# Kernel tuning notes

Hardware: AMD Instinct MI355X
Metric: run time of the kernel (lower is better)

## Reference

```python
import jax, jax.numpy as jnp
import numpy as np

B, N, M, D = 2, 256, 8, 256      # batch, seq, modalities, dmodel
H, DH = 8, 64                     # heads, dim_head (hardcoded defaults)
INNER = H * DH                    # 512
MULT = 4                          # FFN mult
SCALE = DH ** -0.5
EPS = 1e-5


def layer_norm(x, g, b):
    mu = jnp.mean(x, axis=-1, keepdims=True)
    var = jnp.mean((x - mu) ** 2, axis=-1, keepdims=True)
    return (x - mu) * jax.lax.rsqrt(var + EPS) * g + b


def setup_inputs() -> dict:
    key = jax.random.key(0)
    ks = jax.random.split(key, 8)
    s = 0.02
    return {
        "x": jax.random.normal(ks[0], (B, D, M, N), jnp.float32),
        "Wq": jax.random.normal(ks[1], (D, INNER), jnp.float32) * s,
        "Wkv": jax.random.normal(ks[2], (D, 2 * INNER), jnp.float32) * s,
        "Wout": jax.random.normal(ks[3], (INNER * M, D * M), jnp.float32) * s,
        "bout": jnp.zeros((D * M,), jnp.float32),
        "g1": jnp.ones((D,), jnp.float32),
        "beta1": jnp.zeros((D,), jnp.float32),
        "Wff1": jax.random.normal(ks[4], (D, 2 * D * MULT), jnp.float32) * s,
        "bff1": jnp.zeros((2 * D * MULT,), jnp.float32),
        "Wff2": jax.random.normal(ks[5], (D * MULT, D), jnp.float32) * s,
        "bff2": jnp.zeros((D,), jnp.float32),
        "g2": jnp.ones((D,), jnp.float32),
        "beta2": jnp.zeros((D,), jnp.float32),
    }


def reference(x, Wq, Wkv, Wout, bout, g1, beta1, Wff1, bff1, Wff2, bff2, g2, beta2):
    x_shape = x.shape
    xt = jnp.transpose(x, (0, 3, 2, 1))          # [B,N,M,D]
    # --- Channel_Seq_Big_Attention (self-attention, context = x) ---
    q = (xt @ Wq).reshape(B, N, M, H, DH)
    kv = xt @ Wkv
    k, v = jnp.split(kv, 2, axis=-1)
    k = k.reshape(B, N, M, H, DH)
    v = v.reshape(B, N, M, H, DH)
    # sim: [(b h), i, j, m, z] kept as [B,H,i,j,m,z]
    sim = jnp.einsum('bimhd,bjzhd->bhijmz', q, k) * SCALE
    attn = jax.nn.softmax(sim, axis=2)           # softmax over j (dim=-3 of bijmz)
    out = jnp.einsum('bhijmz,bjmhd->bizhd', attn, v)  # [B,N,M,H,DH]
    out = out.reshape(B, N, M * H * DH)          # 'b n (m h d)'
    o = (out @ Wout + bout).reshape(B, N, M, D)
    # --- residual + post-norm ---
    xt = layer_norm(xt + o, g1, beta1)
    # --- GEGLU FFN ---
    hg = xt @ Wff1 + bff1
    a, gate = jnp.split(hg, 2, axis=-1)
    ff = (a * jax.nn.gelu(gate, approximate=False)) @ Wff2 + bff2
    xt = layer_norm(xt + ff, g2, beta2)
    return xt.reshape(x_shape)                   # torch .view(x_shape)
```

## Files before the change

### kernel.cpp

```cpp
#include <hip/hip_runtime.h>
#include <math.h>

#define SCALE_ 0.125f
#define KS_ 0.1803368801111244f

typedef __attribute__((ext_vector_type(8))) short bf16x8;
typedef __attribute__((ext_vector_type(4))) short bf16x4;
typedef __attribute__((ext_vector_type(4))) float f32x4;

__device__ inline short f2bf(float f) {
  unsigned u = __builtin_bit_cast(unsigned, f);
  u += 0x7fff + ((u >> 16) & 1);
  return (short)(u >> 16);
}

__global__ __launch_bounds__(256) void k_transpose(const float* __restrict__ x, float* __restrict__ xt,
                                                   short* __restrict__ xtbf) {
  __shared__ float tile[32][33];
  int bm = blockIdx.z; int b = bm >> 3; int m = bm & 7;
  int d0 = blockIdx.x * 32, n0 = blockIdx.y * 32;
#pragma unroll
  for (int r = 0; r < 32; r += 8) {
    int d = d0 + threadIdx.y + r, n = n0 + threadIdx.x;
    tile[threadIdx.y + r][threadIdx.x] = x[((size_t)(b * 256 + d) * 8 + m) * 256 + n];
  }
  __syncthreads();
#pragma unroll
  for (int r = 0; r < 32; r += 8) {
    int n = n0 + threadIdx.y + r, d = d0 + threadIdx.x;
    float v = tile[threadIdx.x][threadIdx.y + r];
    size_t idx = ((size_t)(b * 256 + n) * 8 + m) * 256 + d;
    xt[idx] = v;
    xtbf[idx] = f2bf(v);
  }
}

__global__ __launch_bounds__(256) void k_wt(const float* __restrict__ W, short* __restrict__ WT, int K, int N) {
  __shared__ float tile[32][33];
  int n0 = blockIdx.x * 32, k0 = blockIdx.y * 32;
  int tx = threadIdx.x & 31, ty = threadIdx.x >> 5;
#pragma unroll
  for (int r = 0; r < 32; r += 8)
    tile[ty + r][tx] = W[(size_t)(k0 + ty + r) * N + n0 + tx];
  __syncthreads();
#pragma unroll
  for (int r = 0; r < 32; r += 8)
    WT[(size_t)(n0 + ty + r) * K + k0 + tx] = f2bf(tile[tx][ty + r]);
}

__global__ __launch_bounds__(256) void k_gemm_bf(const short* __restrict__ A, const short* __restrict__ Bt,
                                                 const float* __restrict__ bias, float* __restrict__ C,
                                                 int M, int N, int K, int Ks) {
  __shared__ short As[64 * 40];
  __shared__ short Bs[64 * 40];
  int t = threadIdx.x;
  int row0 = blockIdx.y * 64, col0 = blockIdx.x * 64;
  int kp = blockIdx.z;
  int kbeg = kp * Ks, kend = kbeg + Ks;
  int w = t >> 6, lane = t & 63, quad = lane >> 4, l16 = lane & 15;
  int wr = w >> 1, wc = w & 1;
  int lrow = t >> 2, lch = (t & 3) * 8;
  const short* Ap = A + (size_t)(row0 + lrow) * K + lch;
  const short* Bp = Bt + (size_t)(col0 + lrow) * K + lch;
  f32x4 acc[2][2] = {{{0,0,0,0},{0,0,0,0}},{{0,0,0,0},{0,0,0,0}}};
  bf16x8 av = *(const bf16x8*)(Ap + kbeg);
  bf16x8 bv = *(const bf16x8*)(Bp + kbeg);
  for (int k0 = kbeg; k0 < kend; k0 += 32) {
    *(bf16x8*)&As[lrow * 40 + lch] = av;
    *(bf16x8*)&Bs[lrow * 40 + lch] = bv;
    __syncthreads();
    if (k0 + 32 < kend) {
      av = *(const bf16x8*)(Ap + k0 + 32);
      bv = *(const bf16x8*)(Bp + k0 + 32);
    }
    bf16x8 af[2], bf[2];
#pragma unroll
    for (int rf = 0; rf < 2; rf++) af[rf] = *(const bf16x8*)&As[(wr * 32 + rf * 16 + l16) * 40 + quad * 8];
#pragma unroll
    for (int cf = 0; cf < 2; cf++) bf[cf] = *(const bf16x8*)&Bs[(wc * 32 + cf * 16 + l16) * 40 + quad * 8];
#pragma unroll
    for (int rf = 0; rf < 2; rf++)
#pragma unroll
      for (int cf = 0; cf < 2; cf++)
        acc[rf][cf] = __builtin_amdgcn_mfma_f32_16x16x32_bf16(af[rf], bf[cf], acc[rf][cf], 0, 0, 0);
    __syncthreads();
  }
  float* Cp = C + (size_t)kp * M * N;
#pragma unroll
  for (int rf = 0; rf < 2; rf++)
#pragma unroll
    for (int cf = 0; cf < 2; cf++) {
      int col = col0 + wc * 32 + cf * 16 + l16;
      float vb = (bias && kp == 0) ? bias[col] : 0.0f;
#pragma unroll
      for (int r = 0; r < 4; r++) {
        int row = row0 + wr * 32 + rf * 16 + quad * 4 + r;
        Cp[(size_t)row * N + col] = acc[rf][cf][r] + vb;
      }
    }
}

__global__ __launch_bounds__(256) void k_prep_qfrag(const float* __restrict__ q, short* __restrict__ qfrag) {
  int c = blockIdx.x * 256 + threadIdx.x;
  int lane = c & 63, ks = (c >> 6) & 1, rt = (c >> 7) & 127, bh = c >> 14;
  int b = bh >> 3, h = bh & 7;
  int m = rt >> 4, i = ((rt & 15) << 4) + (lane & 15);
  int d = ks * 32 + (lane >> 4) * 8;
  const float* src = q + (size_t)((b * 256 + i) * 8 + m) * 512 + h * 64 + d;
  float4 f0 = *(const float4*)src, f1 = *(const float4*)(src + 4);
  bf16x8 o;
  o[0] = f2bf(f0.x); o[1] = f2bf(f0.y); o[2] = f2bf(f0.z); o[3] = f2bf(f0.w);
  o[4] = f2bf(f1.x); o[5] = f2bf(f1.y); o[6] = f2bf(f1.z); o[7] = f2bf(f1.w);
  *(bf16x8*)(qfrag + (size_t)c * 8) = o;
}

__global__ __launch_bounds__(256) void k_prep_kfrag(const float* __restrict__ kv, short* __restrict__ kfrag) {
  int c = blockIdx.x * 256 + threadIdx.x;
  int lane = c & 63, ks = (c >> 6) & 1, rt = (c >> 7) & 127, bh = c >> 14;
  int b = bh >> 3, h = bh & 7;
  int z = rt >> 4, j = ((rt & 15) << 4) + (lane & 15);
  int d = ks * 32 + (lane >> 4) * 8;
  const float* src = kv + (size_t)((b * 256 + j) * 8 + z) * 1024 + h * 64 + d;
  float4 f0 = *(const float4*)src, f1 = *(const float4*)(src + 4);
  bf16x8 o;
  o[0] = f2bf(f0.x); o[1] = f2bf(f0.y); o[2] = f2bf(f0.z); o[3] = f2bf(f0.w);
  o[4] = f2bf(f1.x); o[5] = f2bf(f1.y); o[6] = f2bf(f1.z); o[7] = f2bf(f1.w);
  *(bf16x8*)(kfrag + (size_t)c * 8) = o;
}

__global__ __launch_bounds__(256) void k_prep_vfrag(const float* __restrict__ kv, short* __restrict__ vfrag) {
  __shared__ float Vs[256 * 66];
  int jc = blockIdx.x, bh = blockIdx.y;
  int b = bh >> 3, h = bh & 7;
  int t = threadIdx.x;
#pragma unroll
  for (int cc = 0; cc < 16; cc++) {
    int c = cc * 256 + t;
    int row = c >> 4, ch = c & 15;
    int m = row >> 5, jl = row & 31;
    float4 f = *(const float4*)(kv + (size_t)((b * 256 + jc * 32 + jl) * 8 + m) * 1024 + 512 + h * 64 + ch * 4);
    *(float4*)&Vs[row * 66 + ch * 4] = f;
  }
  __syncthreads();
  int m0 = t >> 6, lane = t & 63, quad = lane >> 4, l16 = lane & 15;
#pragma unroll
  for (int dt = 0; dt < 4; dt++)
#pragma unroll
    for (int jf = 0; jf < 2; jf++) {
      bf16x8 o;
#pragma unroll
      for (int e = 0; e < 8; e++) {
        int row = (2 * m0 + (e >> 2)) * 32 + jf * 16 + quad * 4 + (e & 3);
        o[e] = f2bf(Vs[row * 66 + dt * 16 + l16]);
      }
      size_t cid = ((((size_t)(bh * 8 + jc) * 4 + m0) * 4 + dt) * 2 + jf) * 64 + lane;
      *(bf16x8*)(vfrag + cid * 8) = o;
    }
}

__global__ __launch_bounds__(256) void k_attn_den4(const short* __restrict__ qfrag, const short* __restrict__ kfrag,
                                                   float* __restrict__ rdg) {
  int ct = blockIdx.x, mp = blockIdx.y, bh = blockIdx.z;
  int t = threadIdx.x;
  int w = t >> 6, lane = t & 63;
  bf16x8 bfr[2];
#pragma unroll
  for (int ks = 0; ks < 2; ks++)
    bfr[ks] = *(const bf16x8*)(kfrag + ((size_t)((bh * 128 + ct * 4 + w) * 2 + ks)) * 512 + lane * 8);
  for (int mi = 0; mi < 4; mi++) {
    int m = mp * 4 + mi;
    float facc = 0.0f;
#pragma unroll 4
    for (int it2 = 0; it2 < 16; it2++) {
      const short* ap = qfrag + ((size_t)((bh * 128 + m * 16 + it2) * 2)) * 512 + lane * 8;
      bf16x8 a0 = *(const bf16x8*)ap;
      bf16x8 a1 = *(const bf16x8*)(ap + 512);
      f32x4 c = {0, 0, 0, 0};
      c = __builtin_amdgcn_mfma_f32_16x16x32_bf16(a0, bfr[0], c, 0, 0, 0);
      c = __builtin_amdgcn_mfma_f32_16x16x32_bf16(a1, bfr[1], c, 0, 0, 0);
#pragma unroll
      for (int r = 0; r < 4; r++) facc += __builtin_amdgcn_exp2f(c[r] * KS_);
    }
    facc += __shfl_xor(facc, 16);
    facc += __shfl_xor(facc, 32);
    if (lane < 16)
      rdg[(size_t)(bh * 8 + m) * 2048 + ct * 64 + w * 16 + lane] = -__builtin_amdgcn_logf(facc);
  }
}

__global__ __launch_bounds__(256) void k_attn_out4(const short* __restrict__ qfrag, const short* __restrict__ kfrag,
                                                   const short* __restrict__ vfrag, const float* __restrict__ rdg,
                                                   short* __restrict__ ao) {
  __shared__ float red[4 * 64 * 17];
  int z = blockIdx.x, it = blockIdx.y, bh = blockIdx.z;
  int b = bh >> 3, h = bh & 7;
  int i0 = it * 16;
  int t = threadIdx.x, w = t >> 6, lane = t & 63, quad = lane >> 4, l16 = lane & 15;
  const float* rb = rdg + (size_t)bh * 16384;
  bf16x8 qf[2][2];
#pragma unroll
  for (int mm = 0; mm < 2; mm++)
#pragma unroll
    for (int ks = 0; ks < 2; ks++)
      qf[mm][ks] = *(const bf16x8*)(qfrag + ((size_t)((bh * 128 + (2 * w + mm) * 16 + it) * 2 + ks)) * 512 + lane * 8);
  f32x4 acc[4] = {{0,0,0,0},{0,0,0,0},{0,0,0,0},{0,0,0,0}};
  for (int jc = 0; jc < 8; jc++) {
    bf16x8 vf[4][2];
#pragma unroll
    for (int dt = 0; dt < 4; dt++)
#pragma unroll
      for (int jf = 0; jf < 2; jf++)
        vf[dt][jf] = *(const bf16x8*)(vfrag + ((((size_t)(bh * 8 + jc) * 4 + w) * 4 + dt) * 2 + jf) * 512 + lane * 8);
    f32x4 c[2][2] = {{{0,0,0,0},{0,0,0,0}},{{0,0,0,0},{0,0,0,0}}};
#pragma unroll
    for (int jf = 0; jf < 2; jf++) {
      const short* kp = kfrag + ((size_t)((bh * 128 + z * 16 + jc * 2 + jf) * 2)) * 512 + lane * 8;
      bf16x8 k0 = *(const bf16x8*)kp;
      bf16x8 k1 = *(const bf16x8*)(kp + 512);
#pragma unroll
      for (int mm = 0; mm < 2; mm++) {
        c[jf][mm] = __builtin_amdgcn_mfma_f32_16x16x32_bf16(k0, qf[mm][0], c[jf][mm], 0, 0, 0);
        c[jf][mm] = __builtin_amdgcn_mfma_f32_16x16x32_bf16(k1, qf[mm][1], c[jf][mm], 0, 0, 0);
      }
    }
    bf16x8 pf[2];
#pragma unroll
    for (int jf = 0; jf < 2; jf++) {
      float4 nv0 = *(const float4*)(rb + (size_t)(2 * w) * 2048 + z * 256 + jc * 32 + jf * 16 + quad * 4);
      float4 nv1 = *(const float4*)(rb + (size_t)(2 * w + 1) * 2048 + z * 256 + jc * 32 + jf * 16 + quad * 4);
      float n0[4] = {nv0.x, nv0.y, nv0.z, nv0.w};
      float n1[4] = {nv1.x, nv1.y, nv1.z, nv1.w};
      unsigned u[8];
#pragma unroll
      for (int e = 0; e < 4; e++) {
        u[e]     = __builtin_bit_cast(unsigned, __builtin_amdgcn_exp2f(fmaf(c[jf][0][e], KS_, n0[e]))) + 0x8000u;
        u[e + 4] = __builtin_bit_cast(unsigned, __builtin_amdgcn_exp2f(fmaf(c[jf][1][e], KS_, n1[e]))) + 0x8000u;
      }
      uint4 pv;
      pv.x = __builtin_amdgcn_perm(u[1], u[0], 0x07060302u);
      pv.y = __builtin_amdgcn_perm(u[3], u[2], 0x07060302u);
      pv.z = __builtin_amdgcn_perm(u[5], u[4], 0x07060302u);
      pv.w = __builtin_amdgcn_perm(u[7], u[6], 0x07060302u);
      pf[jf] = __builtin_bit_cast(bf16x8, pv);
    }
#pragma unroll
    for (int dt = 0; dt < 4; dt++)
#pragma unroll
      for (int jf = 0; jf < 2; jf++)
        acc[dt] = __builtin_amdgcn_mfma_f32_16x16x32_bf16(vf[dt][jf], pf[jf], acc[dt], 0, 0, 0);
  }
#pragma unroll
  for (int dt = 0; dt < 4; dt++)
#pragma unroll
    for (int r = 0; r < 4; r++)
      red[w * 1088 + (dt * 16 + quad * 4 + r) * 17 + l16] = acc[dt][r];
  __syncthreads();
  {
    int i = t >> 4, dg = t & 15;
    float s[4] = {0, 0, 0, 0};
#pragma unroll
    for (int w2 = 0; w2 < 4; w2++)
#pragma unroll
      for (int r2 = 0; r2 < 4; r2++)
        s[r2] += red[w2 * 1088 + (dg * 4 + r2) * 17 + i];
    bf16x4 ov;
#pragma unroll
    for (int r2 = 0; r2 < 4; r2++) ov[r2] = f2bf(s[r2]);
    *(bf16x4*)(ao + (size_t)((b * 256 + i0 + i) * 8 + z) * 512 + h * 64 + dg * 4) = ov;
  }
}

__global__ __launch_bounds__(256) void k_ln(const float* __restrict__ X, const float* __restrict__ P, int np,
                                            const float* __restrict__ g, const float* __restrict__ be,
                                            float* __restrict__ Y, short* __restrict__ Ybf) {
  __shared__ float sm[8];
  int row = blockIdx.x, t = threadIdx.x;
  int lane = t & 63, w = t >> 6;
  size_t base = (size_t)row * 256;
  float v = X[base + t];
  for (int p = 0; p < np; p++) v += P[(size_t)p * 1048576 + base + t];
  float s = v;
  s += __shfl_xor(s, 1); s += __shfl_xor(s, 2); s += __shfl_xor(s, 4);
  s += __shfl_xor(s, 8); s += __shfl_xor(s, 16); s += __shfl_xor(s, 32);
  if (lane == 0) sm[w] = s;
  __syncthreads();
  float mu = (sm[0] + sm[1] + sm[2] + sm[3]) * (1.0f / 256.0f);
  float dv = v - mu;
  float s2 = dv * dv;
  s2 += __shfl_xor(s2, 1); s2 += __shfl_xor(s2, 2); s2 += __shfl_xor(s2, 4);
  s2 += __shfl_xor(s2, 8); s2 += __shfl_xor(s2, 16); s2 += __shfl_xor(s2, 32);
  if (lane == 0) sm[4 + w] = s2;
  __syncthreads();
  float var = (sm[4] + sm[5] + sm[6] + sm[7]) * (1.0f / 256.0f);
  float rs = rsqrtf(var + 1e-5f);
  float res = dv * rs * g[t] + be[t];
  Y[base + t] = res;
  if (Ybf) Ybf[base + t] = f2bf(res);
}

__global__ __launch_bounds__(256) void k_geglu(const float* __restrict__ hg, short* __restrict__ gg) {
  int idx = blockIdx.x * 256 + threadIdx.x;
  int r = idx >> 8, c4 = (idx & 255) * 4;
  float4 a = *(const float4*)&hg[(size_t)r * 2048 + c4];
  float4 gt = *(const float4*)&hg[(size_t)r * 2048 + 1024 + c4];
  float av[4] = {a.x, a.y, a.z, a.w};
  float gv[4] = {gt.x, gt.y, gt.z, gt.w};
  bf16x4 o;
#pragma unroll
  for (int e = 0; e < 4; e++) {
    float ge = 0.5f * gv[e] * (1.0f + erff(gv[e] * 0.70710678118654752f));
    o[e] = f2bf(av[e] * ge);
  }
  *(bf16x4*)(gg + (size_t)r * 1024 + c4) = o;
}

extern "C" void kernel_launch(void* const* d_in, const int* in_sizes, int n_in,
                              void* d_out, int out_size, void* d_ws, size_t ws_size,
                              hipStream_t stream) {
  const float* x    = (const float*)d_in[0];
  const float* Wq   = (const float*)d_in[1];
  const float* Wkv  = (const float*)d_in[2];
  const float* Wout = (const float*)d_in[3];
  const float* bout = (const float*)d_in[4];
  const float* g1   = (const float*)d_in[5];
  const float* be1  = (const float*)d_in[6];
  const float* Wff1 = (const float*)d_in[7];
  const float* bff1 = (const float*)d_in[8];
  const float* Wff2 = (const float*)d_in[9];
  const float* bff2 = (const float*)d_in[10];
  const float* g2   = (const float*)d_in[11];
  const float* be2  = (const float*)d_in[12];
  float* out = (float*)d_out;
  float* w = (float*)d_ws;

  float* xt   = w;
  float* q    = w + 1048576;
  float* kv   = w + 3145728;
  float* part = w + 1048576;
  float* hg   = w + 1048576;
  float* y    = w + 9437184;
  float* rdg  = w + 11534336;
  short* sb     = (short*)(w + 11796480);
  short* qfrag  = sb;
  short* kfrag  = sb + 2097152;
  short* vfrag  = sb + 4194304;
  short* xt_bf  = sb + 6291456;
  short* ao_bf  = sb + 7340032;
  short* y_bf   = sb + 9437184;
  short* gg_bf  = sb + 10485760;
  short* WqT    = sb + 14680064;
  short* WkvT   = sb + 14811136;
  short* WoutT  = sb + 15073280;
  short* Wff1T  = sb + 23461888;
  short* Wff2T  = sb + 23986176;

  k_transpose<<<dim3(8, 8, 16), dim3(32, 8), 0, stream>>>(x, xt, xt_bf);
  k_wt<<<dim3(16, 8), 256, 0, stream>>>(Wq, WqT, 256, 512);
  k_wt<<<dim3(32, 8), 256, 0, stream>>>(Wkv, WkvT, 256, 1024);
  k_wt<<<dim3(64, 128), 256, 0, stream>>>(Wout, WoutT, 4096, 2048);
  k_wt<<<dim3(64, 8), 256, 0, stream>>>(Wff1, Wff1T, 256, 2048);
  k_wt<<<dim3(8, 32), 256, 0, stream>>>(Wff2, Wff2T, 1024, 256);
  k_gemm_bf<<<dim3(8, 64, 1), 256, 0, stream>>>(xt_bf, WqT, nullptr, q, 4096, 512, 256, 256);
  k_gemm_bf<<<dim3(16, 64, 1), 256, 0, stream>>>(xt_bf, WkvT, nullptr, kv, 4096, 1024, 256, 256);
  k_prep_qfrag<<<1024, 256, 0, stream>>>(q, qfrag);
  k_prep_kfrag<<<1024, 256, 0, stream>>>(kv, kfrag);
  k_prep_vfrag<<<dim3(8, 16), 256, 0, stream>>>(kv, vfrag);
  k_attn_den4<<<dim3(32, 2, 16), 256, 0, stream>>>(qfrag, kfrag, rdg);
  k_attn_out4<<<dim3(8, 16, 16), 256, 0, stream>>>(qfrag, kfrag, vfrag, rdg, ao_bf);
  k_gemm_bf<<<dim3(32, 8, 4), 256, 0, stream>>>(ao_bf, WoutT, bout, part, 512, 2048, 4096, 1024);
  k_ln<<<4096, 256, 0, stream>>>(xt, part, 4, g1, be1, y, y_bf);
  k_gemm_bf<<<dim3(32, 64, 1), 256, 0, stream>>>(y_bf, Wff1T, bff1, hg, 4096, 2048, 256, 256);
  k_geglu<<<4096, 256, 0, stream>>>(hg, gg_bf);
  k_gemm_bf<<<dim3(4, 64, 4), 256, 0, stream>>>(gg_bf, Wff2T, bff2, part, 4096, 256, 1024, 256);
  k_ln<<<4096, 256, 0, stream>>>(y, part, 4, g2, be2, out, nullptr);
}
```

Measured before the change: 264.9 us.

## Fuse QKV GEMMs, fuse GEGLU into FF1 GEMM, retile attention kernels

Concatenates the transposed Wq and Wkv so a single GEMM produces a packed qkv buffer, and the fragment-prep kernels now read from that layout. Adds a GEMM that computes the value and gate columns together and applies bias and erf-GELU in its epilogue, so the fp32 hg intermediate and the separate GEGLU kernel are gone. The attention denominator kernel now handles two key tiles per wave, and the output kernel handles two query tiles per block, reusing loaded K and V fragments. The trade is more registers per thread and fewer blocks, which can lower occupancy.

```diff
diff --git a/kernel.cpp b/kernel.cpp
--- a/kernel.cpp
+++ b/kernel.cpp
@@ -1,7 +1,6 @@
 #include <hip/hip_runtime.h>
 #include <math.h>
 
-#define SCALE_ 0.125f
 #define KS_ 0.1803368801111244f
 
 typedef __attribute__((ext_vector_type(8))) short bf16x8;
@@ -100,13 +99,76 @@
     }
 }
 
-__global__ __launch_bounds__(256) void k_prep_qfrag(const float* __restrict__ q, short* __restrict__ qfrag) {
+__global__ __launch_bounds__(256) void k_ff1g(const short* __restrict__ A, const short* __restrict__ Bt,
+                                              const float* __restrict__ bias, short* __restrict__ gg) {
+  __shared__ short As[64 * 40];
+  __shared__ short Ba[64 * 40];
+  __shared__ short Bg[64 * 40];
+  int t = threadIdx.x;
+  int colA0 = blockIdx.x * 64, row0 = blockIdx.y * 64;
+  int w = t >> 6, lane = t & 63, quad = lane >> 4, l16 = lane & 15;
+  int wr = w >> 1, wc = w & 1;
+  int lrow = t >> 2, lch = (t & 3) * 8;
+  const short* Ap  = A + (size_t)(row0 + lrow) * 256 + lch;
+  const short* Bpa = Bt + (size_t)(colA0 + lrow) * 256 + lch;
+  const short* Bpg = Bt + (size_t)(1024 + colA0 + lrow) * 256 + lch;
+  f32x4 za = {0, 0, 0, 0};
+  f32x4 acc_a[2][2] = {{za, za}, {za, za}};
+  f32x4 acc_g[2][2] = {{za, za}, {za, za}};
+  bf16x8 av = *(const bf16x8*)(Ap);
+  bf16x8 bva = *(const bf16x8*)(Bpa);
+  bf16x8 bvg = *(const bf16x8*)(Bpg);
+  for (int k0 = 0; k0 < 256; k0 += 32) {
+    *(bf16x8*)&As[lrow * 40 + lch] = av;
+    *(bf16x8*)&Ba[lrow * 40 + lch] = bva;
+    *(bf16x8*)&Bg[lrow * 40 + lch] = bvg;
+    __syncthreads();
+    if (k0 + 32 < 256) {
+      av  = *(const bf16x8*)(Ap + k0 + 32);
+      bva = *(const bf16x8*)(Bpa + k0 + 32);
+      bvg = *(const bf16x8*)(Bpg + k0 + 32);
+    }
+    bf16x8 af[2], ba[2], bg[2];
+#pragma unroll
+    for (int rf = 0; rf < 2; rf++) af[rf] = *(const bf16x8*)&As[(wr * 32 + rf * 16 + l16) * 40 + quad * 8];
+#pragma unroll
+    for (int cf = 0; cf < 2; cf++) {
+      ba[cf] = *(const bf16x8*)&Ba[(wc * 32 + cf * 16 + l16) * 40 + quad * 8];
+      bg[cf] = *(const bf16x8*)&Bg[(wc * 32 + cf * 16 + l16) * 40 + quad * 8];
+    }
+#pragma unroll
+    for (int rf = 0; rf < 2; rf++)
+#pragma unroll
+      for (int cf = 0; cf < 2; cf++) {
+        acc_a[rf][cf] = __builtin_amdgcn_mfma_f32_16x16x32_bf16(af[rf], ba[cf], acc_a[rf][cf], 0, 0, 0);
+        acc_g[rf][cf] = __builtin_amdgcn_mfma_f32_16x16x32_bf16(af[rf], bg[cf], acc_g[rf][cf], 0, 0, 0);
+      }
+    __syncthreads();
+  }
+#pragma unroll
+  for (int rf = 0; rf < 2; rf++)
+#pragma unroll
+    for (int cf = 0; cf < 2; cf++) {
+      int col = colA0 + wc * 32 + cf * 16 + l16;
+      float ba_ = bias[col], bg_ = bias[1024 + col];
+#pragma unroll
+      for (int r = 0; r < 4; r++) {
+        int row = row0 + wr * 32 + rf * 16 + quad * 4 + r;
+        float a = acc_a[rf][cf][r] + ba_;
+        float g = acc_g[rf][cf][r] + bg_;
+        float ge = 0.5f * g * (1.0f + erff(g * 0.70710678118654752f));
+        gg[(size_t)row * 1024 + col] = f2bf(a * ge);
+      }
+    }
+}
+
+__global__ __launch_bounds__(256) void k_prep_qfrag(const float* __restrict__ qkv, short* __restrict__ qfrag) {
   int c = blockIdx.x * 256 + threadIdx.x;
   int lane = c & 63, ks = (c >> 6) & 1, rt = (c >> 7) & 127, bh = c >> 14;
   int b = bh >> 3, h = bh & 7;
   int m = rt >> 4, i = ((rt & 15) << 4) + (lane & 15);
   int d = ks * 32 + (lane >> 4) * 8;
-  const float* src = q + (size_t)((b * 256 + i) * 8 + m) * 512 + h * 64 + d;
+  const float* src = qkv + (size_t)((b * 256 + i) * 8 + m) * 1536 + h * 64 + d;
   float4 f0 = *(const float4*)src, f1 = *(const float4*)(src + 4);
   bf16x8 o;
   o[0] = f2bf(f0.x); o[1] = f2bf(f0.y); o[2] = f2bf(f0.z); o[3] = f2bf(f0.w);
@@ -114,13 +176,13 @@
   *(bf16x8*)(qfrag + (size_t)c * 8) = o;
 }
 
-__global__ __launch_bounds__(256) void k_prep_kfrag(const float* __restrict__ kv, short* __restrict__ kfrag) {
+__global__ __launch_bounds__(256) void k_prep_kfrag(const float* __restrict__ qkv, short* __restrict__ kfrag) {
   int c = blockIdx.x * 256 + threadIdx.x;
   int lane = c & 63, ks = (c >> 6) & 1, rt = (c >> 7) & 127, bh = c >> 14;
   int b = bh >> 3, h = bh & 7;
   int z = rt >> 4, j = ((rt & 15) << 4) + (lane & 15);
   int d = ks * 32 + (lane >> 4) * 8;
-  const float* src = kv + (size_t)((b * 256 + j) * 8 + z) * 1024 + h * 64 + d;
+  const float* src = qkv + (size_t)((b * 256 + j) * 8 + z) * 1536 + 512 + h * 64 + d;
   float4 f0 = *(const float4*)src, f1 = *(const float4*)(src + 4);
   bf16x8 o;
   o[0] = f2bf(f0.x); o[1] = f2bf(f0.y); o[2] = f2bf(f0.z); o[3] = f2bf(f0.w);
@@ -128,7 +190,7 @@
   *(bf16x8*)(kfrag + (size_t)c * 8) = o;
 }
 
-__global__ __launch_bounds__(256) void k_prep_vfrag(const float* __restrict__ kv, short* __restrict__ vfrag) {
+__global__ __launch_bounds__(256) void k_prep_vfrag(const float* __restrict__ qkv, short* __restrict__ vfrag) {
   __shared__ float Vs[256 * 66];
   int jc = blockIdx.x, bh = blockIdx.y;
   int b = bh >> 3, h = bh & 7;
@@ -138,7 +200,7 @@
     int c = cc * 256 + t;
     int row = c >> 4, ch = c & 15;
     int m = row >> 5, jl = row & 31;
-    float4 f = *(const float4*)(kv + (size_t)((b * 256 + jc * 32 + jl) * 8 + m) * 1024 + 512 + h * 64 + ch * 4);
+    float4 f = *(const float4*)(qkv + (size_t)((b * 256 + jc * 32 + jl) * 8 + m) * 1536 + 1024 + h * 64 + ch * 4);
     *(float4*)&Vs[row * 66 + ch * 4] = f;
   }
   __syncthreads();
@@ -158,52 +220,69 @@
     }
 }
 
-__global__ __launch_bounds__(256) void k_attn_den4(const short* __restrict__ qfrag, const short* __restrict__ kfrag,
+__global__ __launch_bounds__(256) void k_attn_den5(const short* __restrict__ qfrag, const short* __restrict__ kfrag,
                                                    float* __restrict__ rdg) {
-  int ct = blockIdx.x, mp = blockIdx.y, bh = blockIdx.z;
+  int ct2 = blockIdx.x, mp = blockIdx.y, bh = blockIdx.z;
   int t = threadIdx.x;
   int w = t >> 6, lane = t & 63;
-  bf16x8 bfr[2];
-#pragma unroll
-  for (int ks = 0; ks < 2; ks++)
-    bfr[ks] = *(const bf16x8*)(kfrag + ((size_t)((bh * 128 + ct * 4 + w) * 2 + ks)) * 512 + lane * 8);
-  for (int mi = 0; mi < 4; mi++) {
-    int m = mp * 4 + mi;
-    float facc = 0.0f;
+  int rt0 = ct2 * 8 + w * 2;
+  bf16x8 bfr[2][2];
+#pragma unroll
+  for (int cf = 0; cf < 2; cf++)
+#pragma unroll
+    for (int ks = 0; ks < 2; ks++)
+      bfr[cf][ks] = *(const bf16x8*)(kfrag + ((size_t)((bh * 128 + rt0 + cf) * 2 + ks)) * 512 + lane * 8);
+  for (int mi = 0; mi < 2; mi++) {
+    int m = mp * 2 + mi;
+    float fa0 = 0.0f, fa1 = 0.0f;
 #pragma unroll 4
     for (int it2 = 0; it2 < 16; it2++) {
       const short* ap = qfrag + ((size_t)((bh * 128 + m * 16 + it2) * 2)) * 512 + lane * 8;
       bf16x8 a0 = *(const bf16x8*)ap;
       bf16x8 a1 = *(const bf16x8*)(ap + 512);
-      f32x4 c = {0, 0, 0, 0};
-      c = __builtin_amdgcn_mfma_f32_16x16x32_bf16(a0, bfr[0], c, 0, 0, 0);
-      c = __builtin_amdgcn_mfma_f32_16x16x32_bf16(a1, bfr[1], c, 0, 0, 0);
-#pragma unroll
-      for (int r = 0; r < 4; r++) facc += __builtin_amdgcn_exp2f(c[r] * KS_);
-    }
-    facc += __shfl_xor(facc, 16);
-    facc += __shfl_xor(facc, 32);
-    if (lane < 16)
-      rdg[(size_t)(bh * 8 + m) * 2048 + ct * 64 + w * 16 + lane] = -__builtin_amdgcn_logf(facc);
-  }
-}
-
-__global__ __launch_bounds__(256) void k_attn_out4(const short* __restrict__ qfrag, const short* __restrict__ kfrag,
+      f32x4 c0 = {0, 0, 0, 0}, c1 = {0, 0, 0, 0};
+      c0 = __builtin_amdgcn_mfma_f32_16x16x32_bf16(a0, bfr[0][0], c0, 0, 0, 0);
+      c0 = __builtin_amdgcn_mfma_f32_16x16x32_bf16(a1, bfr[0][1], c0, 0, 0, 0);
+      c1 = __builtin_amdgcn_mfma_f32_16x16x32_bf16(a0, bfr[1][0], c1, 0, 0, 0);
+      c1 = __builtin_amdgcn_mfma_f32_16x16x32_bf16(a1, bfr[1][1], c1, 0, 0, 0);
+#pragma unroll
+      for (int r = 0; r < 4; r++) {
+        fa0 += __builtin_amdgcn_exp2f(c0[r] * KS_);
+        fa1 += __builtin_amdgcn_exp2f(c1[r] * KS_);
+      }
+    }
+    fa0 += __shfl_xor(fa0, 16); fa0 += __shfl_xor(fa0, 32);
+    fa1 += __shfl_xor(fa1, 16); fa1 += __shfl_xor(fa1, 32);
+    if (lane < 16) {
+      rdg[(size_t)(bh * 8 + m) * 2048 + rt0 * 16 + lane] = -__builtin_amdgcn_logf(fa0);
+      rdg[(size_t)(bh * 8 + m) * 2048 + (rt0 + 1) * 16 + lane] = -__builtin_amdgcn_logf(fa1);
+    }
+  }
+}
+
+__global__ __launch_bounds__(256) void k_attn_out5(const short* __restrict__ qfrag, const short* __restrict__ kfrag,
                                                    const short* __restrict__ vfrag, const float* __restrict__ rdg,
                                                    short* __restrict__ ao) {
   __shared__ float red[4 * 64 * 17];
-  int z = blockIdx.x, it = blockIdx.y, bh = blockIdx.z;
+  int z = blockIdx.x, itp = blockIdx.y, bh = blockIdx.z;
   int b = bh >> 3, h = bh & 7;
-  int i0 = it * 16;
   int t = threadIdx.x, w = t >> 6, lane = t & 63, quad = lane >> 4, l16 = lane & 15;
   const float* rb = rdg + (size_t)bh * 16384;
-  bf16x8 qf[2][2];
-#pragma unroll
-  for (int mm = 0; mm < 2; mm++)
-#pragma unroll
-    for (int ks = 0; ks < 2; ks++)
-      qf[mm][ks] = *(const bf16x8*)(qfrag + ((size_t)((bh * 128 + (2 * w + mm) * 16 + it) * 2 + ks)) * 512 + lane * 8);
-  f32x4 acc[4] = {{0,0,0,0},{0,0,0,0},{0,0,0,0},{0,0,0,0}};
+  f32x4 z4 = {0, 0, 0, 0};
+  bf16x8 qf[2][2][2];
+#pragma unroll
+  for (int iti = 0; iti < 2; iti++)
+#pragma unroll
+    for (int mm = 0; mm < 2; mm++)
+#pragma unroll
+      for (int ks = 0; ks < 2; ks++)
+        qf[iti][mm][ks] = *(const bf16x8*)(qfrag +
+            ((size_t)((bh * 128 + (2 * w + mm) * 16 + itp * 2 + iti) * 2 + ks)) * 512 + lane * 8);
+  f32x4 acc[2][4];
+#pragma unroll
+  for (int iti = 0; iti < 2; iti++)
+#pragma unroll
+    for (int dt = 0; dt < 4; dt++) acc[iti][dt] = z4;
   for (int jc = 0; jc < 8; jc++) {
     bf16x8 vf[4][2];
 #pragma unroll
@@ -211,62 +290,75 @@
 #pragma unroll
       for (int jf = 0; jf < 2; jf++)
         vf[dt][jf] = *(const bf16x8*)(vfrag + ((((size_t)(bh * 8 + jc) * 4 + w) * 4 + dt) * 2 + jf) * 512 + lane * 8);
-    f32x4 c[2][2] = {{{0,0,0,0},{0,0,0,0}},{{0,0,0,0},{0,0,0,0}}};
+    bf16x8 kf[2][2];
 #pragma unroll
     for (int jf = 0; jf < 2; jf++) {
       const short* kp = kfrag + ((size_t)((bh * 128 + z * 16 + jc * 2 + jf) * 2)) * 512 + lane * 8;
-      bf16x8 k0 = *(const bf16x8*)kp;
-      bf16x8 k1 = *(const bf16x8*)(kp + 512);
-#pragma unroll
-      for (int mm = 0; mm < 2; mm++) {
-        c[jf][mm] = __builtin_amdgcn_mfma_f32_16x16x32_bf16(k0, qf[mm][0], c[jf][mm], 0, 0, 0);
-        c[jf][mm] = __builtin_amdgcn_mfma_f32_16x16x32_bf16(k1, qf[mm][1], c[jf][mm], 0, 0, 0);
-      }
-    }
-    bf16x8 pf[2];
+      kf[jf][0] = *(const bf16x8*)kp;
+      kf[jf][1] = *(const bf16x8*)(kp + 512);
+    }
+    float n0[2][4], n1[2][4];
 #pragma unroll
     for (int jf = 0; jf < 2; jf++) {
       float4 nv0 = *(const float4*)(rb + (size_t)(2 * w) * 2048 + z * 256 + jc * 32 + jf * 16 + quad * 4);
       float4 nv1 = *(const float4*)(rb + (size_t)(2 * w + 1) * 2048 + z * 256 + jc * 32 + jf * 16 + quad * 4);
-      float n0[4] = {nv0.x, nv0.y, nv0.z, nv0.w};
-      float n1[4] = {nv1.x, nv1.y, nv1.z, nv1.w};
-      unsigned u[8];
-#pragma unroll
-      for (int e = 0; e < 4; e++) {
-        u[e]     = __builtin_bit_cast(unsigned, __builtin_amdgcn_exp2f(fmaf(c[jf][0][e], KS_, n0[e]))) + 0x8000u;
-        u[e + 4] = __builtin_bit_cast(unsigned, __builtin_amdgcn_exp2f(fmaf(c[jf][1][e], KS_, n1[e]))) + 0x8000u;
-      }
-      uint4 pv;
-      pv.x = __builtin_amdgcn_perm(u[1], u[0], 0x07060302u);
-      pv.y = __builtin_amdgcn_perm(u[3], u[2], 0x07060302u);
-      pv.z = __builtin_amdgcn_perm(u[5], u[4], 0x07060302u);
-      pv.w = __builtin_amdgcn_perm(u[7], u[6], 0x07060302u);
-      pf[jf] = __builtin_bit_cast(bf16x8, pv);
-    }
+      n0[jf][0] = nv0.x; n0[jf][1] = nv0.y; n0[jf][2] = nv0.z; n0[jf][3] = nv0.w;
+      n1[jf][0] = nv1.x; n1[jf][1] = nv1.y; n1[jf][2] = nv1.z; n1[jf][3] = nv1.w;
+    }
+#pragma unroll
+    for (int iti = 0; iti < 2; iti++) {
+      f32x4 c[2][2] = {{z4, z4}, {z4, z4}};
+#pragma unroll
+      for (int jf = 0; jf < 2; jf++)
+#pragma unroll
+        for (int mm = 0; mm < 2; mm++) {
+          c[jf][mm] = __builtin_amdgcn_mfma_f32_16x16x32_bf16(kf[jf][0], qf[iti][mm][0], c[jf][mm], 0, 0, 0);
+          c[jf][mm] = __builtin_amdgcn_mfma_f32_16x16x32_bf16(kf[jf][1], qf[iti][mm][1], c[jf][mm], 0, 0, 0);
+        }
+      bf16x8 pf[2];
+#pragma unroll
+      for (int jf = 0; jf < 2; jf++) {
+        unsigned u[8];
+#pragma unroll
+        for (int e = 0; e < 4; e++) {
+          u[e]     = __builtin_bit_cast(unsigned, __builtin_amdgcn_exp2f(fmaf(c[jf][0][e], KS_, n0[jf][e]))) + 0x8000u;
+          u[e + 4] = __builtin_bit_cast(unsigned, __builtin_amdgcn_exp2f(fmaf(c[jf][1][e], KS_, n1[jf][e]))) + 0x8000u;
+        }
+        uint4 pv;
+        pv.x = __builtin_amdgcn_perm(u[1], u[0], 0x07060302u);
+        pv.y = __builtin_amdgcn_perm(u[3], u[2], 0x07060302u);
+        pv.z = __builtin_amdgcn_perm(u[5], u[4], 0x07060302u);
+        pv.w = __builtin_amdgcn_perm(u[7], u[6], 0x07060302u);
+        pf[jf] = __builtin_bit_cast(bf16x8, pv);
+      }
+#pragma unroll
+      for (int dt = 0; dt < 4; dt++)
+#pragma unroll
+        for (int jf = 0; jf < 2; jf++)
+          acc[iti][dt] = __builtin_amdgcn_mfma_f32_16x16x32_bf16(vf[dt][jf], pf[jf], acc[iti][dt], 0, 0, 0);
+    }
+  }
+  for (int iti = 0; iti < 2; iti++) {
 #pragma unroll
     for (int dt = 0; dt < 4; dt++)
 #pragma unroll
-      for (int jf = 0; jf < 2; jf++)
-        acc[dt] = __builtin_amdgcn_mfma_f32_16x16x32_bf16(vf[dt][jf], pf[jf], acc[dt], 0, 0, 0);
-  }
-#pragma unroll
-  for (int dt = 0; dt < 4; dt++)
-#pragma unroll
-    for (int r = 0; r < 4; r++)
-      red[w * 1088 + (dt * 16 + quad * 4 + r) * 17 + l16] = acc[dt][r];
-  __syncthreads();
-  {
-    int i = t >> 4, dg = t & 15;
-    float s[4] = {0, 0, 0, 0};
-#pragma unroll
-    for (int w2 = 0; w2 < 4; w2++)
-#pragma unroll
-      for (int r2 = 0; r2 < 4; r2++)
-        s[r2] += red[w2 * 1088 + (dg * 4 + r2) * 17 + i];
-    bf16x4 ov;
-#pragma unroll
-    for (int r2 = 0; r2 < 4; r2++) ov[r2] = f2bf(s[r2]);
-    *(bf16x4*)(ao + (size_t)((b * 256 + i0 + i) * 8 + z) * 512 + h * 64 + dg * 4) = ov;
+      for (int r = 0; r < 4; r++)
+        red[w * 1088 + (dt * 16 + quad * 4 + r) * 17 + l16] = acc[iti][dt][r];
+    __syncthreads();
+    {
+      int i = t >> 4, dg = t & 15;
+      float s[4] = {0, 0, 0, 0};
+#pragma unroll
+      for (int w2 = 0; w2 < 4; w2++)
+#pragma unroll
+        for (int r2 = 0; r2 < 4; r2++)
+          s[r2] += red[w2 * 1088 + (dg * 4 + r2) * 17 + i];
+      bf16x4 ov;
+#pragma unroll
+      for (int r2 = 0; r2 < 4; r2++) ov[r2] = f2bf(s[r2]);
+      *(bf16x4*)(ao + (size_t)((b * 256 + itp * 32 + iti * 16 + i) * 8 + z) * 512 + h * 64 + dg * 4) = ov;
+    }
+    __syncthreads();
   }
 }
 
@@ -298,22 +390,6 @@
   if (Ybf) Ybf[base + t] = f2bf(res);
 }
 
-__global__ __launch_bounds__(256) void k_geglu(const float* __restrict__ hg, short* __restrict__ gg) {
-  int idx = blockIdx.x * 256 + threadIdx.x;
-  int r = idx >> 8, c4 = (idx & 255) * 4;
-  float4 a = *(const float4*)&hg[(size_t)r * 2048 + c4];
-  float4 gt = *(const float4*)&hg[(size_t)r * 2048 + 1024 + c4];
-  float av[4] = {a.x, a.y, a.z, a.w};
-  float gv[4] = {gt.x, gt.y, gt.z, gt.w};
-  bf16x4 o;
-#pragma unroll
-  for (int e = 0; e < 4; e++) {
-    float ge = 0.5f * gv[e] * (1.0f + erff(gv[e] * 0.70710678118654752f));
-    o[e] = f2bf(av[e] * ge);
-  }
-  *(bf16x4*)(gg + (size_t)r * 1024 + c4) = o;
-}
-
 extern "C" void kernel_launch(void* const* d_in, const int* in_sizes, int n_in,
                               void* d_out, int out_size, void* d_ws, size_t ws_size,
                               hipStream_t stream) {
@@ -334,10 +410,8 @@
   float* w = (float*)d_ws;
 
   float* xt   = w;
-  float* q    = w + 1048576;
-  float* kv   = w + 3145728;
+  float* qkv  = w + 1048576;
   float* part = w + 1048576;
-  float* hg   = w + 1048576;
   float* y    = w + 9437184;
   float* rdg  = w + 11534336;
   short* sb     = (short*)(w + 11796480);
@@ -348,29 +422,26 @@
   short* ao_bf  = sb + 7340032;
   short* y_bf   = sb + 9437184;
   short* gg_bf  = sb + 10485760;
-  short* WqT    = sb + 14680064;
-  short* WkvT   = sb + 14811136;
+  short* WqkvT  = sb + 14680064;
   short* WoutT  = sb + 15073280;
   short* Wff1T  = sb + 23461888;
   short* Wff2T  = sb + 23986176;
 
   k_transpose<<<dim3(8, 8, 16), dim3(32, 8), 0, stream>>>(x, xt, xt_bf);
-  k_wt<<<dim3(16, 8), 256, 0, stream>>>(Wq, WqT, 256, 512);
-  k_wt<<<dim3(32, 8), 256, 0, stream>>>(Wkv, WkvT, 256, 1024);
+  k_wt<<<dim3(16, 8), 256, 0, stream>>>(Wq, WqkvT, 256, 512);
+  k_wt<<<dim3(32, 8), 256, 0, stream>>>(Wkv, WqkvT + 131072, 256, 1024);
   k_wt<<<dim3(64, 128), 256, 0, stream>>>(Wout, WoutT, 4096, 2048);
   k_wt<<<dim3(64, 8), 256, 0, stream>>>(Wff1, Wff1T, 256, 2048);
   k_wt<<<dim3(8, 32), 256, 0, stream>>>(Wff2, Wff2T, 1024, 256);
-  k_gemm_bf<<<dim3(8, 64, 1), 256, 0, stream>>>(xt_bf, WqT, nullptr, q, 4096, 512, 256, 256);
-  k_gemm_bf<<<dim3(16, 64, 1), 256, 0, stream>>>(xt_bf, WkvT, nullptr, kv, 4096, 1024, 256, 256);
-  k_prep_qfrag<<<1024, 256, 0, stream>>>(q, qfrag);
-  k_prep_kfrag<<<1024, 256, 0, stream>>>(kv, kfrag);
-  k_prep_vfrag<<<dim3(8, 16), 256, 0, stream>>>(kv, vfrag);
-  k_attn_den4<<<dim3(32, 2, 16), 256, 0, stream>>>(qfrag, kfrag, rdg);
-  k_attn_out4<<<dim3(8, 16, 16), 256, 0, stream>>>(qfrag, kfrag, vfrag, rdg, ao_bf);
+  k_gemm_bf<<<dim3(24, 64, 1), 256, 0, stream>>>(xt_bf, WqkvT, nullptr, qkv, 4096, 1536, 256, 256);
+  k_prep_qfrag<<<1024, 256, 0, stream>>>(qkv, qfrag);
+  k_prep_kfrag<<<1024, 256, 0, stream>>>(qkv, kfrag);
+  k_prep_vfrag<<<dim3(8, 16), 256, 0, stream>>>(qkv, vfrag);
+  k_attn_den5<<<dim3(16, 4, 16), 256, 0, stream>>>(qfrag, kfrag, rdg);
+  k_attn_out5<<<dim3(8, 8, 16), 256, 0, stream>>>(qfrag, kfrag, vfrag, rdg, ao_bf);
   k_gemm_bf<<<dim3(32, 8, 4), 256, 0, stream>>>(ao_bf, WoutT, bout, part, 512, 2048, 4096, 1024);
   k_ln<<<4096, 256, 0, stream>>>(xt, part, 4, g1, be1, y, y_bf);
-  k_gemm_bf<<<dim3(32, 64, 1), 256, 0, stream>>>(y_bf, Wff1T, bff1, hg, 4096, 2048, 256, 256);
-  k_geglu<<<4096, 256, 0, stream>>>(hg, gg_bf);
+  k_ff1g<<<dim3(16, 64), 256, 0, stream>>>(y_bf, Wff1T, bff1, gg_bf);
   k_gemm_bf<<<dim3(4, 64, 4), 256, 0, stream>>>(gg_bf, Wff2T, bff2, part, 4096, 256, 1024, 256);
   k_ln<<<4096, 256, 0, stream>>>(y, part, 4, g2, be2, out, nullptr);
 }
```

Result: faster. 239.3 us (-9.7%).
